# Optimization experiments

Hardware: AMD Instinct MI355X
Metric: run time of the kernel (lower is better)

The kernel has to match this reference:

```python
import jax, jax.numpy as jnp
import numpy as np
from jax import lax

DN = ('NCHW', 'OIHW', 'NCHW')


def convbn(x, w, s, b, relu=True):
    # conv (no bias) + folded BatchNorm affine (+ optional ReLU)
    y = lax.conv_general_dilated(x, w, (1, 1), 'SAME', dimension_numbers=DN)
    y = y * s[None, :, None, None] + b[None, :, None, None]
    return jnp.maximum(y, 0.0) if relu else y


_PARAM_SHAPES = [
    ('t', (128, 256, 3, 3)), ('l', (128, 256, 3, 3)),
    ('b', (128, 256, 3, 3)), ('r', (128, 256, 3, 3)),
    ('tl3', (256, 128, 3, 3)), ('br3', (256, 128, 3, 3)),
    ('tl1', (256, 256, 1, 1)), ('br1', (256, 256, 1, 1)),
    ('tlo', (256, 256, 3, 3)), ('bro', (256, 256, 3, 3)),
]


def setup_inputs() -> dict:
    key = jax.random.key(0)
    B, C, H, W = 8, 256, 128, 128
    ks = jax.random.split(key, 3 * len(_PARAM_SHAPES) + 1)
    inp = {'x': jax.random.normal(ks[0], (B, C, H, W), jnp.float32)}
    i = 1
    for name, shape in _PARAM_SHAPES:
        cout = shape[0]
        inp['w_' + name] = jax.random.normal(ks[i], shape, jnp.float32) * 0.05
        inp['s_' + name] = 1.0 + 0.1 * jax.random.normal(ks[i + 1], (cout,), jnp.float32)
        inp['b_' + name] = 0.1 * jax.random.normal(ks[i + 2], (cout,), jnp.float32)
        i += 3
    return inp


def reference(x, w_t, s_t, b_t, w_l, s_l, b_l, w_b, s_b, b_b, w_r, s_r, b_r,
              w_tl3, s_tl3, b_tl3, w_br3, s_br3, b_br3,
              w_tl1, s_tl1, b_tl1, w_br1, s_br1, b_br1,
              w_tlo, s_tlo, b_tlo, w_bro, s_bro, b_bro):
    # directional corner pools = (reverse-)cummax along H (axis 2) or W (axis 3)
    t = convbn(x, w_t, s_t, b_t)
    tp = lax.cummax(t, axis=2, reverse=True)   # top_pool: max over rows >= h
    l = convbn(x, w_l, s_l, b_l)
    lp = lax.cummax(l, axis=3, reverse=True)   # left_pool: max over cols >= w
    bo = convbn(x, w_b, s_b, b_b)
    bp = lax.cummax(bo, axis=2)                # bottom_pool: max over rows <= h
    r = convbn(x, w_r, s_r, b_r)
    rp = lax.cummax(r, axis=3)                 # right_pool: max over cols <= w

    tl = convbn(tp + lp, w_tl3, s_tl3, b_tl3, relu=False)
    tl = jnp.maximum(tl + convbn(x, w_tl1, s_tl1, b_tl1, relu=False), 0.0)
    out_tl = convbn(tl, w_tlo, s_tlo, b_tlo)

    br = convbn(bp + rp, w_br3, s_br3, b_br3, relu=False)
    br = jnp.maximum(br + convbn(x, w_br1, s_br1, b_br1, relu=False), 0.0)
    out_br = convbn(br, w_bro, s_bro, b_bro)
    return out_tl, out_br
```

## Files before the change

### kernel.cpp

```cpp
#include <hip/hip_runtime.h>
#include <cstdint>
#include <cstddef>


typedef float  f32x4 __attribute__((ext_vector_type(4)));
typedef float  f4v   __attribute__((ext_vector_type(4)));
typedef short  s16x8 __attribute__((ext_vector_type(8)));
typedef unsigned short u16x4 __attribute__((ext_vector_type(4)));

__device__ __forceinline__ float bf2f(unsigned short u) {
    unsigned x = ((unsigned)u) << 16;
    return __builtin_bit_cast(float, x);
}
__device__ __forceinline__ unsigned short f2bf(float f) {
    unsigned u = __builtin_bit_cast(unsigned, f);
    unsigned r = (u + 0x7fffu + ((u >> 16) & 1u)) >> 16;
    return (unsigned short)r;
}

#define GL_LDS(gp, lp) __builtin_amdgcn_global_load_lds( \
    (const __attribute__((address_space(1))) unsigned int*)(const void*)(gp), \
    (__attribute__((address_space(3))) unsigned int*)(void*)(lp), 16, 0, 0)

template<int CIN, int COUT, bool RELU, bool OUTF32, bool SWZ>
__global__ __launch_bounds__(256, 4)
void conv3_mfma(const unsigned short* __restrict__ in,
                const unsigned short* __restrict__ wpk,
                const float* __restrict__ sc, const float* __restrict__ bi,
                void* __restrict__ outv)
{
    __shared__ unsigned short lds[2][8704];
    const int tid  = threadIdx.x;
    const int lane = tid & 63;
    const int wv   = tid >> 6;
    const int c    = lane & 15;
    const int g    = lane >> 4;

    constexpr int GX  = (COUT / 128) * 2;
    int gx, hy, n;
    if (SWZ) {
        constexpr int NWG = GX * 64 * 8;
        constexpr int Q   = NWG / 8;
        const int braw = blockIdx.x + GX * (blockIdx.y + 64 * blockIdx.z);
        const int wl   = (braw & 7) * Q + (braw >> 3);
        gx = wl % GX;
        const int rest = wl / GX;
        hy = rest & 63;
        n  = rest >> 6;
    } else {
        gx = blockIdx.x; hy = blockIdx.y; n = blockIdx.z;
    }
    const int wtile  = gx & 1;
    const int octile = gx >> 1;
    const int h0   = hy * 2;
    const int w0   = wtile * 64;
    const int r    = wv >> 1;
    const int ocbase = octile * 128 + (wv & 1) * 64;
    const int ocf0   = octile * 8 + (wv & 1) * 4;

    int addrB[3];
    #pragma unroll
    for (int kx = 0; kx < 3; ++kx) {
        int ps0 = c + kx;
        addrB[kx] = r * 4224 + ps0 * 64 + ((g ^ ((ps0 >> 1) & 3)) << 4);
    }

    int so[5];
    #pragma unroll
    for (int it = 0; it < 5; ++it) {
        int u   = it * 256 + tid;
        int row = u / 264;
        int rem = u - row * 264;
        int ps  = rem >> 2;
        int s   = rem & 3;
        int icq = s ^ ((ps >> 1) & 3);
        so[it] = ((n * 130 + h0 + row) * 130 + (w0 + ps)) * CIN + icq * 8;
    }

    auto STAGE = [&](int chunk, int bsel) {
        const unsigned short* bp = in + chunk * 32;
        char* lb = (char*)lds + bsel * 17408 + tid * 16;
        #pragma unroll
        for (int it = 0; it < 4; ++it)
            GL_LDS(bp + so[it], lb + it * 4096);
        if (wv == 0)
            GL_LDS(bp + so[4], lb + 16384);
    };

    f32x4 acc[4][4];
    #pragma unroll
    for (int m = 0; m < 4; ++m)
        #pragma unroll
        for (int p = 0; p < 4; ++p) acc[m][p] = 0.0f;

    const int NC = CIN / 32;
    STAGE(0, 0);
    __syncthreads();

    for (int chunk = 0; chunk < NC; ++chunk) {
        const int cur = chunk & 1;
        if (chunk + 1 < NC) STAGE(chunk + 1, cur ^ 1);
        const char* lb = (const char*)lds + cur * 17408;
        #pragma unroll
        for (int kk = 0; kk < 9; ++kk) {
            const int ky = kk / 3, kx = kk % 3;
            s16x8 af[4], bf[4];
            #pragma unroll
            for (int m = 0; m < 4; ++m)
                af[m] = *(const s16x8*)(wpk
                    + ((size_t)((chunk * 9 + kk) * (COUT / 16) + ocf0 + m)) * 512 + lane * 8);
            #pragma unroll
            for (int p = 0; p < 4; ++p)
                bf[p] = *(const s16x8*)(lb + addrB[kx] + ky * 4224 + p * 1024);
            #pragma unroll
            for (int m = 0; m < 4; ++m)
                #pragma unroll
                for (int p = 0; p < 4; ++p)
                    acc[m][p] = __builtin_amdgcn_mfma_f32_16x16x32_bf16(af[m], bf[p], acc[m][p], 0, 0, 0);
        }
        __syncthreads();
    }

    #pragma unroll
    for (int m = 0; m < 4; ++m) {
        const int oc4 = ocbase + m * 16 + g * 4;
        const f4v s4 = *(const f4v*)(sc + oc4);
        const f4v b4 = *(const f4v*)(bi + oc4);
        #pragma unroll
        for (int p = 0; p < 4; ++p) {
            const int w = w0 + p * 16 + c;
            float y[4];
            #pragma unroll
            for (int j = 0; j < 4; ++j) {
                y[j] = acc[m][p][j] * s4[j] + b4[j];
                if (RELU) y[j] = fmaxf(y[j], 0.0f);
            }
            if (OUTF32) {
                float* op = (float*)outv + (((size_t)n * COUT + oc4) << 14) + ((h0 + r) << 7) + w;
                op[0] = y[0]; op[16384] = y[1]; op[32768] = y[2]; op[49152] = y[3];
            } else {
                u16x4 pk;
                #pragma unroll
                for (int j = 0; j < 4; ++j) pk[j] = f2bf(y[j]);
                *(u16x4*)((unsigned short*)outv
                    + ((size_t)(n * 130 + h0 + r + 1) * 130 + w + 1) * COUT + oc4) = pk;
            }
        }
    }
}

__global__ __launch_bounds__(256, 4)
void conv3_tlbr(const unsigned short* __restrict__ in,
                const unsigned short* __restrict__ wq0,
                const float* __restrict__ sA, const float* __restrict__ bA,
                unsigned short* __restrict__ tt0)
{
    __shared__ unsigned short lds[2][8704];
    const int tid  = threadIdx.x;
    const int lane = tid & 63;
    const int wv   = tid >> 6;
    const int c    = lane & 15;
    const int g    = lane >> 4;

    const int b  = blockIdx.x;
    const int x  = b & 7;
    const int t  = b >> 3;
    const int q  = t & 3;
    const int ts = x + 8 * (t >> 2);
    const int wtile = ts & 1;
    const int hy    = (ts >> 1) & 63;
    const int n     = ts >> 7;
    const int h0 = hy * 2;
    const int w0 = wtile * 64;
    const int r  = wv >> 1;
    const int ocbase = (wv & 1) * 64;
    const int ocf0   = (wv & 1) * 4;

    const unsigned short* wpk = wq0 + q * 294912;
    const int outoff = ((q & 1) << 1) | (q >> 1);
    unsigned short* outv = tt0 + (size_t)outoff * ((size_t)8 * 130 * 130 * 128);
    const float* sc = sA + q * 128;
    const float* bi = bA + q * 128;

    int addrB[3];
    #pragma unroll
    for (int kx = 0; kx < 3; ++kx) {
        int ps0 = c + kx;
        addrB[kx] = r * 4224 + ps0 * 64 + ((g ^ ((ps0 >> 1) & 3)) << 4);
    }

    int so[5];
    #pragma unroll
    for (int it = 0; it < 5; ++it) {
        int u   = it * 256 + tid;
        int row = u / 264;
        int rem = u - row * 264;
        int ps  = rem >> 2;
        int s   = rem & 3;
        int icq = s ^ ((ps >> 1) & 3);
        so[it] = ((n * 130 + h0 + row) * 130 + (w0 + ps)) * 256 + icq * 8;
    }

    auto STAGE = [&](int chunk, int bsel) {
        const unsigned short* bp = in + chunk * 32;
        char* lb = (char*)lds + bsel * 17408 + tid * 16;
        #pragma unroll
        for (int it = 0; it < 4; ++it)
            GL_LDS(bp + so[it], lb + it * 4096);
        if (wv == 0)
            GL_LDS(bp + so[4], lb + 16384);
    };

    f32x4 acc[4][4];
    #pragma unroll
    for (int m = 0; m < 4; ++m)
        #pragma unroll
        for (int p = 0; p < 4; ++p) acc[m][p] = 0.0f;

    STAGE(0, 0);
    __syncthreads();

    for (int chunk = 0; chunk < 8; ++chunk) {
        const int cur = chunk & 1;
        if (chunk + 1 < 8) STAGE(chunk + 1, cur ^ 1);
        const char* lb = (const char*)lds + cur * 17408;
        #pragma unroll
        for (int kk = 0; kk < 9; ++kk) {
            const int ky = kk / 3, kx = kk % 3;
            s16x8 af[4], bf[4];
            #pragma unroll
            for (int m = 0; m < 4; ++m)
                af[m] = *(const s16x8*)(wpk
                    + ((size_t)((chunk * 9 + kk) * 8 + ocf0 + m)) * 512 + lane * 8);
            #pragma unroll
            for (int p = 0; p < 4; ++p)
                bf[p] = *(const s16x8*)(lb + addrB[kx] + ky * 4224 + p * 1024);
            #pragma unroll
            for (int m = 0; m < 4; ++m)
                #pragma unroll
                for (int p = 0; p < 4; ++p)
                    acc[m][p] = __builtin_amdgcn_mfma_f32_16x16x32_bf16(af[m], bf[p], acc[m][p], 0, 0, 0);
        }
        __syncthreads();
    }

    #pragma unroll
    for (int m = 0; m < 4; ++m) {
        const int oc4 = ocbase + m * 16 + g * 4;
        const f4v s4 = *(const f4v*)(sc + oc4);
        const f4v b4 = *(const f4v*)(bi + oc4);
        #pragma unroll
        for (int p = 0; p < 4; ++p) {
            const int w = w0 + p * 16 + c;
            u16x4 pk;
            #pragma unroll
            for (int j = 0; j < 4; ++j)
                pk[j] = f2bf(fmaxf(acc[m][p][j] * s4[j] + b4[j], 0.0f));
            *(u16x4*)(outv + ((size_t)(n * 130 + h0 + r + 1) * 130 + w + 1) * 128 + oc4) = pk;
        }
    }
}

__global__ __launch_bounds__(256, 2)
void conv1_mfma(const unsigned short* __restrict__ xb,
                const unsigned short* __restrict__ w1pk,
                const float* __restrict__ sc, const float* __restrict__ bi,
                unsigned short* __restrict__ io)
{
    const int tid  = threadIdx.x;
    const int h    = blockIdx.y;
    const int n    = blockIdx.z;
    const int lane = tid & 63;
    const int wv   = tid >> 6;
    const int c    = lane & 15;
    const int g    = lane >> 4;
    const int pixbase = (wv >> 1) * 64;
    const int ocbase  = blockIdx.x * 128 + (wv & 1) * 64;
    const int ocf0    = blockIdx.x * 8 + (wv & 1) * 4;
    const size_t pixrow = ((size_t)(n * 130 + h + 1) * 130 + (pixbase + c + 1)) * 256;

    f32x4 acc[4][4];
    #pragma unroll
    for (int m = 0; m < 4; ++m)
        #pragma unroll
        for (int p = 0; p < 4; ++p) acc[m][p] = 0.0f;

    s16x8 a0[4], b0[4], a1[4], b1[4];

#define LOADC(ck, A, B) do {                                                        \
    _Pragma("unroll") for (int p = 0; p < 4; ++p)                                   \
        B[p] = *(const s16x8*)(xb + pixrow + (size_t)(16 * p) * 256 + (ck) * 32 + g * 8); \
    _Pragma("unroll") for (int m = 0; m < 4; ++m)                                   \
        A[m] = *(const s16x8*)(w1pk + ((size_t)((ck) * 16 + ocf0 + m)) * 512 + lane * 8); \
} while (0)
#define MM(A, B)                                                                    \
    _Pragma("unroll") for (int m = 0; m < 4; ++m)                                   \
        _Pragma("unroll") for (int p = 0; p < 4; ++p)                               \
            acc[m][p] = __builtin_amdgcn_mfma_f32_16x16x32_bf16(A[m], B[p], acc[m][p], 0, 0, 0)

    LOADC(0, a0, b0);
    #pragma unroll
    for (int ck = 0; ck < 8; ++ck) {
        if ((ck & 1) == 0) { if (ck < 7) LOADC(ck + 1, a1, b1); MM(a0, b0); }
        else               { if (ck < 7) LOADC(ck + 1, a0, b0); MM(a1, b1); }
    }
#undef LOADC
#undef MM

    #pragma unroll
    for (int m = 0; m < 4; ++m) {
        const int oc4 = ocbase + m * 16 + g * 4;
        const f4v s4 = *(const f4v*)(sc + oc4);
        const f4v b4 = *(const f4v*)(bi + oc4);
        #pragma unroll
        for (int p = 0; p < 4; ++p) {
            const int pix = pixbase + p * 16 + c;
            size_t idx = ((size_t)(n * 130 + h + 1) * 130 + pix + 1) * 256 + oc4;
            u16x4 old = *(const u16x4*)(io + idx);
            u16x4 pk;
            #pragma unroll
            for (int j = 0; j < 4; ++j) {
                float y = acc[m][p][j] * s4[j] + b4[j] + bf2f(old[j]);
                pk[j] = f2bf(fmaxf(y, 0.0f));
            }
            *(u16x4*)(io + idx) = pk;
        }
    }
}

__global__ __launch_bounds__(128)
void pool_h2_k(unsigned short* __restrict__ ta, unsigned short* __restrict__ tb)
{
    const int sel = blockIdx.x & 1;
    const int col = blockIdx.x >> 1;
    unsigned short* p = sel ? tb : ta;
    const int n = col >> 7, w = col & 127, cth = threadIdx.x;
    unsigned short* base = p + (((size_t)n * 130 + 1) * 130 + (w + 1)) * 128 + cth;
    const int stride = 130 * 128;
    float m = -3.402823466e+38f;
    if (sel == 0) {
        for (int gq = 0; gq < 16; ++gq) {
            const int h0 = 127 - gq * 8;
            float v[8];
            #pragma unroll
            for (int j = 0; j < 8; ++j) v[j] = bf2f(base[(size_t)(h0 - j) * stride]);
            unsigned short o[8];
            #pragma unroll
            for (int j = 0; j < 8; ++j) { m = fmaxf(m, v[j]); o[j] = f2bf(m); }
            #pragma unroll
            for (int j = 0; j < 8; ++j) base[(size_t)(h0 - j) * stride] = o[j];
        }
    } else {
        for (int gq = 0; gq < 16; ++gq) {
            const int h0 = gq * 8;
            float v[8];
            #pragma unroll
            for (int j = 0; j < 8; ++j) v[j] = bf2f(base[(size_t)(h0 + j) * stride]);
            unsigned short o[8];
            #pragma unroll
            for (int j = 0; j < 8; ++j) { m = fmaxf(m, v[j]); o[j] = f2bf(m); }
            #pragma unroll
            for (int j = 0; j < 8; ++j) base[(size_t)(h0 + j) * stride] = o[j];
        }
    }
}

__global__ __launch_bounds__(128)
void pool_w_add2_k(const unsigned short* __restrict__ la, unsigned short* __restrict__ ta,
                   const unsigned short* __restrict__ lb, unsigned short* __restrict__ tb)
{
    const int sel = blockIdx.x & 1;
    const int row = blockIdx.x >> 1;
    const unsigned short* ls = sel ? lb : la;
    unsigned short* td = sel ? tb : ta;
    const int n = row >> 7, hh = row & 127, cth = threadIdx.x;
    const size_t rowbase = ((size_t)(n * 130 + hh + 1) * 130) * 128 + cth;
    float m = -3.402823466e+38f;
    if (sel == 0) {
        for (int gq = 0; gq < 16; ++gq) {
            const int w0 = 127 - gq * 8;
            float lv[8], tv[8];
            #pragma unroll
            for (int j = 0; j < 8; ++j) {
                size_t off = rowbase + (size_t)(w0 - j + 1) * 128;
                lv[j] = bf2f(ls[off]); tv[j] = bf2f(td[off]);
            }
            unsigned short o[8];
            #pragma unroll
            for (int j = 0; j < 8; ++j) { m = fmaxf(m, lv[j]); o[j] = f2bf(m + tv[j]); }
            #pragma unroll
            for (int j = 0; j < 8; ++j) td[rowbase + (size_t)(w0 - j + 1) * 128] = o[j];
        }
    } else {
        for (int gq = 0; gq < 16; ++gq) {
            const int w0 = gq * 8;
            float lv[8], tv[8];
            #pragma unroll
            for (int j = 0; j < 8; ++j) {
                size_t off = rowbase + (size_t)(w0 + j + 1) * 128;
                lv[j] = bf2f(ls[off]); tv[j] = bf2f(td[off]);
            }
            unsigned short o[8];
            #pragma unroll
            for (int j = 0; j < 8; ++j) { m = fmaxf(m, lv[j]); o[j] = f2bf(m + tv[j]); }
            #pragma unroll
            for (int j = 0; j < 8; ++j) td[rowbase + (size_t)(w0 + j + 1) * 128] = o[j];
        }
    }
}

__global__ __launch_bounds__(256)
void padzero_k(unsigned short* __restrict__ t, int C)
{
    int idx = blockIdx.x * 256 + threadIdx.x;
    int n = blockIdx.y;
    int cpu = C >> 3;
    if (idx >= 516 * cpu) return;
    int cell = idx / cpu, cq = idx - cell * cpu;
    int h, w;
    if (cell < 260) { h = (cell < 130) ? -1 : 128; w = (cell % 130) - 1; }
    else { int j = cell - 260; w = (j < 128) ? -1 : 128; h = j & 127; }
    size_t off = (((size_t)n * 130 + h + 1) * 130 + (w + 1)) * C + cq * 8;
    uint4 z; z.x = 0; z.y = 0; z.z = 0; z.w = 0;
    *(uint4*)(t + off) = z;
}

__global__ __launch_bounds__(256)
void padzero_all_k(unsigned short* xb, unsigned short* tt, unsigned short* bb,
                   unsigned short* ll, unsigned short* rr)
{
    const int id = blockIdx.y;
    unsigned short* t = id == 0 ? xb : (id == 1 ? tt : (id == 2 ? bb : (id == 3 ? ll : rr)));
    const int C = id == 0 ? 256 : 128;
    int idx = blockIdx.x * 256 + threadIdx.x;
    int n = blockIdx.z;
    int cpu = C >> 3;
    if (idx >= 516 * cpu) return;
    int cell = idx / cpu, cq = idx - cell * cpu;
    int h, w;
    if (cell < 260) { h = (cell < 130) ? -1 : 128; w = (cell % 130) - 1; }
    else { int j = cell - 260; w = (j < 128) ? -1 : 128; h = j & 127; }
    size_t off = (((size_t)n * 130 + h + 1) * 130 + (w + 1)) * C + cq * 8;
    uint4 z; z.x = 0; z.y = 0; z.z = 0; z.w = 0;
    *(uint4*)(t + off) = z;
}

__global__ __launch_bounds__(256)
void transform_x_k(const float* __restrict__ x, unsigned short* __restrict__ xb)
{
    __shared__ float sm[64][132];
    const int h = blockIdx.x, n = blockIdx.y, t = threadIdx.x;
    for (int cc0 = 0; cc0 < 256; cc0 += 64) {
        __syncthreads();
        {
            int ci = t >> 7, wi = t & 127;
            #pragma unroll 8
            for (int k = 0; k < 32; ++k)
                sm[ci + 2 * k][wi] = x[((size_t)(n * 256 + cc0 + ci + 2 * k) << 14) + (h << 7) + wi];
        }
        __syncthreads();
        {
            int wi = t >> 1, cq = t & 1;
            unsigned short tmp[32];
            #pragma unroll
            for (int m2 = 0; m2 < 32; ++m2) tmp[m2] = f2bf(sm[cq * 32 + m2][wi]);
            unsigned short* dst = xb + (((size_t)n * 130 + h + 1) * 130 + wi + 1) * 256 + cc0 + cq * 32;
            #pragma unroll
            for (int q = 0; q < 4; ++q) *(uint4*)(dst + q * 8) = *(const uint4*)(tmp + q * 8);
        }
    }
}

struct PrepArgs {
    const float* w[10];
    unsigned short* dst[10];
    const float* sv[4];
    const float* bv[4];
    float* sA; float* bA;
};

__global__ __launch_bounds__(256)
void prepack_all_k(PrepArgs a)
{
    const int id = blockIdx.y;
    int idx = blockIdx.x * 256 + threadIdx.x;
    if (id == 10) {
        if (idx < 512) {
            a.sA[idx] = a.sv[idx >> 7][idx & 127];
            a.bA[idx] = a.bv[idx >> 7][idx & 127];
        }
        return;
    }
    if (id >= 8) {
        if (idx >= 65536) return;
        int ic = idx & 255, oc = idx >> 8;
        float v = a.w[id][oc * 256 + ic];
        int chunk = ic >> 5, icr = ic & 31, gg = icr >> 3, j = icr & 7;
        int m = oc >> 4, ocr = oc & 15, ln = gg * 16 + ocr;
        a.dst[id][((size_t)(chunk * 16 + m)) * 512 + ln * 8 + j] = f2bf(v);
        return;
    }
    const int CIN  = (id < 4) ? 256 : ((id < 6) ? 128 : 256);
    const int COUT = (id < 4) ? 128 : 256;
    if (idx >= COUT * CIN * 9) return;
    int kk = idx % 9; int rest = idx / 9;
    int ic = rest % CIN; int oc = rest / CIN;
    float v = a.w[id][(size_t)(oc * CIN + ic) * 9 + kk];
    int chunk = ic >> 5, icr = ic & 31, gg = icr >> 3, j = icr & 7;
    int m = oc >> 4, ocr = oc & 15, ln = gg * 16 + ocr;
    a.dst[id][((size_t)((chunk * 9 + kk) * (COUT / 16) + m)) * 512 + ln * 8 + j] = f2bf(v);
}

extern "C" void kernel_launch(void* const* d_in, const int* in_sizes, int n_in,
                              void* d_out, int out_size, void* d_ws, size_t ws_size,
                              hipStream_t stream)
{
    const float* x     = (const float*)d_in[0];
    const float* w_t   = (const float*)d_in[1];
    const float* s_t   = (const float*)d_in[2];
    const float* b_t   = (const float*)d_in[3];
    const float* w_l   = (const float*)d_in[4];
    const float* s_l   = (const float*)d_in[5];
    const float* b_l   = (const float*)d_in[6];
    const float* w_b   = (const float*)d_in[7];
    const float* s_b   = (const float*)d_in[8];
    const float* b_b   = (const float*)d_in[9];
    const float* w_r   = (const float*)d_in[10];
    const float* s_r   = (const float*)d_in[11];
    const float* b_r   = (const float*)d_in[12];
    const float* w_tl3 = (const float*)d_in[13];
    const float* s_tl3 = (const float*)d_in[14];
    const float* b_tl3 = (const float*)d_in[15];
    const float* w_br3 = (const float*)d_in[16];
    const float* s_br3 = (const float*)d_in[17];
    const float* b_br3 = (const float*)d_in[18];
    const float* w_tl1 = (const float*)d_in[19];
    const float* s_tl1 = (const float*)d_in[20];
    const float* b_tl1 = (const float*)d_in[21];
    const float* w_br1 = (const float*)d_in[22];
    const float* s_br1 = (const float*)d_in[23];
    const float* b_br1 = (const float*)d_in[24];
    const float* w_tlo = (const float*)d_in[25];
    const float* s_tlo = (const float*)d_in[26];
    const float* b_tlo = (const float*)d_in[27];
    const float* w_bro = (const float*)d_in[28];
    const float* s_bro = (const float*)d_in[29];
    const float* b_bro = (const float*)d_in[30];

    typedef unsigned short ush;
    const size_t T256 = (size_t)8 * 130 * 130 * 256;
    const size_t T128 = (size_t)8 * 130 * 130 * 128;

    ush* xb = (ush*)d_ws;
    ush* tt = xb + T256;
    ush* bb = tt + T128;
    ush* ll = bb + T128;
    ush* rr = ll + T128;
    ush* wq = rr + T128;
    ush* wp_t   = wq;
    ush* wp_l   = wp_t   + 294912;
    ush* wp_b   = wp_l   + 294912;
    ush* wp_r   = wp_b   + 294912;
    ush* wp_tl3 = wp_r   + 294912;
    ush* wp_br3 = wp_tl3 + 294912;
    ush* wp_tlo = wp_br3 + 294912;
    ush* wp_bro = wp_tlo + 589824;
    ush* wp_tl1 = wp_bro + 589824;
    ush* wp_br1 = wp_tl1 + 65536;
    float* sA   = (float*)(wp_br1 + 65536);
    float* bA   = sA + 512;
    ush* tl = ll;

    PrepArgs pa;
    pa.w[0] = w_t;  pa.w[1] = w_l;  pa.w[2] = w_b;  pa.w[3] = w_r;
    pa.w[4] = w_tl3; pa.w[5] = w_br3; pa.w[6] = w_tlo; pa.w[7] = w_bro;
    pa.w[8] = w_tl1; pa.w[9] = w_br1;
    pa.dst[0] = wp_t;  pa.dst[1] = wp_l;  pa.dst[2] = wp_b;  pa.dst[3] = wp_r;
    pa.dst[4] = wp_tl3; pa.dst[5] = wp_br3; pa.dst[6] = wp_tlo; pa.dst[7] = wp_bro;
    pa.dst[8] = wp_tl1; pa.dst[9] = wp_br1;
    pa.sv[0] = s_t; pa.sv[1] = s_l; pa.sv[2] = s_b; pa.sv[3] = s_r;
    pa.bv[0] = b_t; pa.bv[1] = b_l; pa.bv[2] = b_b; pa.bv[3] = b_r;
    pa.sA = sA; pa.bA = bA;
    prepack_all_k<<<dim3(2304, 11), dim3(256), 0, stream>>>(pa);
    padzero_all_k<<<dim3(516, 5, 8), dim3(256), 0, stream>>>(xb, tt, bb, ll, rr);
    transform_x_k<<<dim3(128, 8), dim3(256), 0, stream>>>(x, xb);

    conv3_tlbr<<<dim3(4096), dim3(256), 0, stream>>>(xb, wp_t, sA, bA, tt);

    pool_h2_k<<<dim3(2048), dim3(128), 0, stream>>>(tt, bb);
    pool_w_add2_k<<<dim3(2048), dim3(128), 0, stream>>>(ll, tt, rr, bb);

    padzero_k<<<dim3(66, 8), dim3(256), 0, stream>>>(tl, 256);
    conv3_mfma<128, 256, false, false, true><<<dim3(4, 64, 8), dim3(256), 0, stream>>>(tt, wp_tl3, s_tl3, b_tl3, tl);
    conv1_mfma<<<dim3(2, 128, 8), dim3(256), 0, stream>>>(xb, wp_tl1, s_tl1, b_tl1, tl);
    conv3_mfma<256, 256, true, true, true><<<dim3(4, 64, 8), dim3(256), 0, stream>>>(tl, wp_tlo, s_tlo, b_tlo, d_out);

    conv3_mfma<128, 256, false, false, true><<<dim3(4, 64, 8), dim3(256), 0, stream>>>(bb, wp_br3, s_br3, b_br3, tl);
    conv1_mfma<<<dim3(2, 128, 8), dim3(256), 0, stream>>>(xb, wp_br1, s_br1, b_br1, tl);
    conv3_mfma<256, 256, true, true, true><<<dim3(4, 64, 8), dim3(256), 0, stream>>>(tl, wp_bro, s_bro, b_bro,
                                                                                     (float*)d_out + 33554432);
}
```

Baseline: 924.8 us.

## Fuse 3x3 and 1x1 residual convs into one kernel for both branches, fold BN scale

Folds the BatchNorm scale into the packed weights and pre-sums the tl3/tl1 and br3/br1 biases, so epilogues only add a bias. The tl3+tl1 and br3+br1 convolutions are merged into a single kernel that accumulates both GEMMs in registers, handles both branches in one launch, and stages the 1x1 input through LDS. The BR intermediate is stored in the output buffer so both branches can run in that one launch. The aim is to drop the read-modify-write of the intermediate, two launches, and the scale loads. The catch is the extra prepack work and relying on the output buffer as scratch being ordered correctly (bro is run first).

```diff
diff --git a/kernel.cpp b/kernel.cpp
--- a/kernel.cpp
+++ b/kernel.cpp
@@ -26,7 +26,7 @@
 __global__ __launch_bounds__(256, 4)
 void conv3_mfma(const unsigned short* __restrict__ in,
                 const unsigned short* __restrict__ wpk,
-                const float* __restrict__ sc, const float* __restrict__ bi,
+                const float* __restrict__ bi,
                 void* __restrict__ outv)
 {
     __shared__ unsigned short lds[2][8704];
@@ -124,7 +124,6 @@
     #pragma unroll
     for (int m = 0; m < 4; ++m) {
         const int oc4 = ocbase + m * 16 + g * 4;
-        const f4v s4 = *(const f4v*)(sc + oc4);
         const f4v b4 = *(const f4v*)(bi + oc4);
         #pragma unroll
         for (int p = 0; p < 4; ++p) {
@@ -132,7 +131,7 @@
             float y[4];
             #pragma unroll
             for (int j = 0; j < 4; ++j) {
-                y[j] = acc[m][p][j] * s4[j] + b4[j];
+                y[j] = acc[m][p][j] + b4[j];
                 if (RELU) y[j] = fmaxf(y[j], 0.0f);
             }
             if (OUTF32) {
@@ -152,7 +151,7 @@
 __global__ __launch_bounds__(256, 4)
 void conv3_tlbr(const unsigned short* __restrict__ in,
                 const unsigned short* __restrict__ wq0,
-                const float* __restrict__ sA, const float* __restrict__ bA,
+                const float* __restrict__ bA,
                 unsigned short* __restrict__ tt0)
 {
     __shared__ unsigned short lds[2][8704];
@@ -179,7 +178,6 @@
     const unsigned short* wpk = wq0 + q * 294912;
     const int outoff = ((q & 1) << 1) | (q >> 1);
     unsigned short* outv = tt0 + (size_t)outoff * ((size_t)8 * 130 * 130 * 128);
-    const float* sc = sA + q * 128;
     const float* bi = bA + q * 128;
 
     int addrB[3];
@@ -247,7 +245,6 @@
     #pragma unroll
     for (int m = 0; m < 4; ++m) {
         const int oc4 = ocbase + m * 16 + g * 4;
-        const f4v s4 = *(const f4v*)(sc + oc4);
         const f4v b4 = *(const f4v*)(bi + oc4);
         #pragma unroll
         for (int p = 0; p < 4; ++p) {
@@ -255,29 +252,99 @@
             u16x4 pk;
             #pragma unroll
             for (int j = 0; j < 4; ++j)
-                pk[j] = f2bf(fmaxf(acc[m][p][j] * s4[j] + b4[j], 0.0f));
+                pk[j] = f2bf(fmaxf(acc[m][p][j] + b4[j], 0.0f));
             *(u16x4*)(outv + ((size_t)(n * 130 + h0 + r + 1) * 130 + w + 1) * 128 + oc4) = pk;
         }
     }
 }
 
-__global__ __launch_bounds__(256, 2)
-void conv1_mfma(const unsigned short* __restrict__ xb,
-                const unsigned short* __restrict__ w1pk,
-                const float* __restrict__ sc, const float* __restrict__ bi,
-                unsigned short* __restrict__ io)
-{
+__global__ __launch_bounds__(256, 4)
+void conv3p1_k(const unsigned short* __restrict__ u0,
+               const unsigned short* __restrict__ xb,
+               const unsigned short* __restrict__ w30,
+               const unsigned short* __restrict__ w10,
+               const float* __restrict__ bsum0,
+               unsigned short* __restrict__ outTL,
+               unsigned short* __restrict__ outBR)
+{
+    __shared__ unsigned short lds[2][8704];
     const int tid  = threadIdx.x;
-    const int h    = blockIdx.y;
-    const int n    = blockIdx.z;
     const int lane = tid & 63;
     const int wv   = tid >> 6;
     const int c    = lane & 15;
     const int g    = lane >> 4;
-    const int pixbase = (wv >> 1) * 64;
-    const int ocbase  = blockIdx.x * 128 + (wv & 1) * 64;
-    const int ocf0    = blockIdx.x * 8 + (wv & 1) * 4;
-    const size_t pixrow = ((size_t)(n * 130 + h + 1) * 130 + (pixbase + c + 1)) * 256;
+
+    const int b  = blockIdx.x;
+    const int x  = b & 7;
+    const int s  = b >> 3;
+    const int q  = s & 1;
+    const int gx = (s >> 1) & 3;
+    const int sp = x + 8 * (s >> 3);
+    const int hy = sp & 63;
+    const int n  = sp >> 6;
+    const int wtile  = gx & 1;
+    const int octile = gx >> 1;
+    const int h0 = hy * 2;
+    const int w0 = wtile * 64;
+    const int r  = wv >> 1;
+    const int ocbase = octile * 128 + (wv & 1) * 64;
+    const int ocf0   = octile * 8 + (wv & 1) * 4;
+
+    const unsigned short* in3 = u0 + (size_t)q * ((size_t)8 * 130 * 130 * 128);
+    const unsigned short* w3  = w30 + q * 294912;
+    const unsigned short* w1  = w10 + q * 65536;
+    const float* bi = bsum0 + q * 256;
+    unsigned short* outv = q ? outBR : outTL;
+
+    int addrB[3];
+    #pragma unroll
+    for (int kx = 0; kx < 3; ++kx) {
+        int ps0 = c + kx;
+        addrB[kx] = r * 4224 + ps0 * 64 + ((g ^ ((ps0 >> 1) & 3)) << 4);
+    }
+    const int addrC1 = r * 4096 + c * 64 + ((g ^ ((c >> 1) & 3)) << 4);
+
+    int so3[5];
+    #pragma unroll
+    for (int it = 0; it < 5; ++it) {
+        int u   = it * 256 + tid;
+        int row = u / 264;
+        int rem = u - row * 264;
+        int ps  = rem >> 2;
+        int ss  = rem & 3;
+        int icq = ss ^ ((ps >> 1) & 3);
+        so3[it] = ((n * 130 + h0 + row) * 130 + (w0 + ps)) * 128 + icq * 8;
+    }
+    int so1[4];
+    #pragma unroll
+    for (int it = 0; it < 4; ++it) {
+        int u   = it * 256 + tid;
+        int sub = u >> 9;
+        int v   = u & 511;
+        int row = v >> 8;
+        int rem = v & 255;
+        int px  = rem >> 2;
+        int ss  = rem & 3;
+        int icq = ss ^ ((px >> 1) & 3);
+        so1[it] = ((n * 130 + h0 + 1 + row) * 130 + (w0 + px + 1)) * 256 + sub * 32 + icq * 8;
+    }
+
+    auto STAGE3 = [&](int chunk, int bsel) {
+        const unsigned short* bp = in3 + chunk * 32;
+        char* lb = (char*)lds + bsel * 17408 + tid * 16;
+        #pragma unroll
+        for (int it = 0; it < 4; ++it)
+            GL_LDS(bp + so3[it], lb + it * 4096);
+        if (wv == 0)
+            GL_LDS(bp + so3[4], lb + 16384);
+    };
+    auto STAGE1 = [&](int j, int bsel) {
+        const unsigned short* bp = xb + j * 64;
+        char* lb = (char*)lds + bsel * 17408 + tid * 16;
+        #pragma unroll
+        for (int it = 0; it < 4; ++it)
+            GL_LDS(bp + so1[it], lb + it * 4096);
+    };
 
     f32x4 acc[4][4];
     #pragma unroll
@@ -285,45 +352,66 @@
         #pragma unroll
         for (int p = 0; p < 4; ++p) acc[m][p] = 0.0f;
 
-    s16x8 a0[4], b0[4], a1[4], b1[4];
-
-#define LOADC(ck, A, B) do {                                                        \
-    _Pragma("unroll") for (int p = 0; p < 4; ++p)                                   \
-        B[p] = *(const s16x8*)(xb + pixrow + (size_t)(16 * p) * 256 + (ck) * 32 + g * 8); \
-    _Pragma("unroll") for (int m = 0; m < 4; ++m)                                   \
-        A[m] = *(const s16x8*)(w1pk + ((size_t)((ck) * 16 + ocf0 + m)) * 512 + lane * 8); \
-} while (0)
-#define MM(A, B)                                                                    \
-    _Pragma("unroll") for (int m = 0; m < 4; ++m)                                   \
-        _Pragma("unroll") for (int p = 0; p < 4; ++p)                               \
-            acc[m][p] = __builtin_amdgcn_mfma_f32_16x16x32_bf16(A[m], B[p], acc[m][p], 0, 0, 0)
-
-    LOADC(0, a0, b0);
-    #pragma unroll
-    for (int ck = 0; ck < 8; ++ck) {
-        if ((ck & 1) == 0) { if (ck < 7) LOADC(ck + 1, a1, b1); MM(a0, b0); }
-        else               { if (ck < 7) LOADC(ck + 1, a0, b0); MM(a1, b1); }
-    }
-#undef LOADC
-#undef MM
+    STAGE3(0, 0);
+    __syncthreads();
+
+    for (int ph = 0; ph < 8; ++ph) {
+        const int cur = ph & 1;
+        if (ph < 3)      STAGE3(ph + 1, cur ^ 1);
+        else if (ph < 7) STAGE1(ph - 3, cur ^ 1);
+        const char* lb = (const char*)lds + cur * 17408;
+        if (ph < 4) {
+            #pragma unroll
+            for (int kk = 0; kk < 9; ++kk) {
+                const int ky = kk / 3, kx = kk % 3;
+                s16x8 af[4], bf[4];
+                #pragma unroll
+                for (int m = 0; m < 4; ++m)
+                    af[m] = *(const s16x8*)(w3
+                        + ((size_t)((ph * 9 + kk) * 16 + ocf0 + m)) * 512 + lane * 8);
+                #pragma unroll
+                for (int p = 0; p < 4; ++p)
+                    bf[p] = *(const s16x8*)(lb + addrB[kx] + ky * 4224 + p * 1024);
+                #pragma unroll
+                for (int m = 0; m < 4; ++m)
+                    #pragma unroll
+                    for (int p = 0; p < 4; ++p)
+                        acc[m][p] = __builtin_amdgcn_mfma_f32_16x16x32_bf16(af[m], bf[p], acc[m][p], 0, 0, 0);
+            }
+        } else {
+            const int j = ph - 4;
+            #pragma unroll
+            for (int sub = 0; sub < 2; ++sub) {
+                s16x8 af[4], bf[4];
+                #pragma unroll
+                for (int m = 0; m < 4; ++m)
+                    af[m] = *(const s16x8*)(w1
+                        + ((size_t)(((j * 2 + sub) * 16) + ocf0 + m)) * 512 + lane * 8);
+                #pragma unroll
+                for (int p = 0; p < 4; ++p)
+                    bf[p] = *(const s16x8*)(lb + sub * 8192 + addrC1 + p * 1024);
+                #pragma unroll
+                for (int m = 0; m < 4; ++m)
+                    #pragma unroll
+                    for (int p = 0; p < 4; ++p)
+                        acc[m][p] = __builtin_amdgcn_mfma_f32_16x16x32_bf16(af[m], bf[p], acc[m][p], 0, 0, 0);
+            }
+        }
+        __syncthreads();
+    }
 
     #pragma unroll
     for (int m = 0; m < 4; ++m) {
         const int oc4 = ocbase + m * 16 + g * 4;
-        const f4v s4 = *(const f4v*)(sc + oc4);
         const f4v b4 = *(const f4v*)(bi + oc4);
         #pragma unroll
         for (int p = 0; p < 4; ++p) {
-            const int pix = pixbase + p * 16 + c;
-            size_t idx = ((size_t)(n * 130 + h + 1) * 130 + pix + 1) * 256 + oc4;
-            u16x4 old = *(const u16x4*)(io + idx);
+            const int w = w0 + p * 16 + c;
             u16x4 pk;
             #pragma unroll
-            for (int j = 0; j < 4; ++j) {
-                float y = acc[m][p][j] * s4[j] + b4[j] + bf2f(old[j]);
-                pk[j] = f2bf(fmaxf(y, 0.0f));
-            }
-            *(u16x4*)(io + idx) = pk;
+            for (int j = 0; j < 4; ++j)
+                pk[j] = f2bf(fmaxf(acc[m][p][j] + b4[j], 0.0f));
+            *(u16x4*)(outv + ((size_t)(n * 130 + h0 + r + 1) * 130 + w + 1) * 256 + oc4) = pk;
         }
     }
 }
@@ -427,11 +515,12 @@
 
 __global__ __launch_bounds__(256)
 void padzero_all_k(unsigned short* xb, unsigned short* tt, unsigned short* bb,
-                   unsigned short* ll, unsigned short* rr)
+                   unsigned short* ll, unsigned short* rr, unsigned short* pbr)
 {
     const int id = blockIdx.y;
-    unsigned short* t = id == 0 ? xb : (id == 1 ? tt : (id == 2 ? bb : (id == 3 ? ll : rr)));
-    const int C = id == 0 ? 256 : 128;
+    unsigned short* t = id == 0 ? xb : (id == 1 ? tt : (id == 2 ? bb :
+                        (id == 3 ? ll : (id == 4 ? rr : pbr))));
+    const int C = (id == 0 || id == 5) ? 256 : 128;
     int idx = blockIdx.x * 256 + threadIdx.x;
     int n = blockIdx.z;
     int cpu = C >> 3;
@@ -474,9 +563,10 @@
 struct PrepArgs {
     const float* w[10];
     unsigned short* dst[10];
-    const float* sv[4];
+    const float* s[10];
     const float* bv[4];
-    float* sA; float* bA;
+    const float* bx[4];
+    float* bA; float* bsum;
 };
 
 __global__ __launch_bounds__(256)
@@ -485,16 +575,15 @@
     const int id = blockIdx.y;
     int idx = blockIdx.x * 256 + threadIdx.x;
     if (id == 10) {
-        if (idx < 512) {
-            a.sA[idx] = a.sv[idx >> 7][idx & 127];
-            a.bA[idx] = a.bv[idx >> 7][idx & 127];
-        }
+        if (idx < 512) a.bA[idx] = a.bv[idx >> 7][idx & 127];
+        else if (idx < 768)  { int i = idx - 512; a.bsum[i]       = a.bx[0][i] + a.bx[1][i]; }
+        else if (idx < 1024) { int i = idx - 768; a.bsum[256 + i] = a.bx[2][i] + a.bx[3][i]; }
         return;
     }
     if (id >= 8) {
         if (idx >= 65536) return;
         int ic = idx & 255, oc = idx >> 8;
-        float v = a.w[id][oc * 256 + ic];
+        float v = a.w[id][oc * 256 + ic] * a.s[id][oc];
         int chunk = ic >> 5, icr = ic & 31, gg = icr >> 3, j = icr & 7;
         int m = oc >> 4, ocr = oc & 15, ln = gg * 16 + ocr;
         a.dst[id][((size_t)(chunk * 16 + m)) * 512 + ln * 8 + j] = f2bf(v);
@@ -505,7 +594,7 @@
     if (idx >= COUT * CIN * 9) return;
     int kk = idx % 9; int rest = idx / 9;
     int ic = rest % CIN; int oc = rest / CIN;
-    float v = a.w[id][(size_t)(oc * CIN + ic) * 9 + kk];
+    float v = a.w[id][(size_t)(oc * CIN + ic) * 9 + kk] * a.s[id][oc];
     int chunk = ic >> 5, icr = ic & 31, gg = icr >> 3, j = icr & 7;
     int m = oc >> 4, ocr = oc & 15, ln = gg * 16 + ocr;
     a.dst[id][((size_t)((chunk * 9 + kk) * (COUT / 16) + m)) * 512 + ln * 8 + j] = f2bf(v);
@@ -567,9 +656,10 @@
     ush* wp_bro = wp_tlo + 589824;
     ush* wp_tl1 = wp_bro + 589824;
     ush* wp_br1 = wp_tl1 + 65536;
-    float* sA   = (float*)(wp_br1 + 65536);
-    float* bA   = sA + 512;
-    ush* tl = ll;
+    float* bA   = (float*)(wp_br1 + 65536);
+    float* bsum = bA + 512;
+    ush* tl  = ll;
+    ush* pbr = (ush*)d_out;
 
     PrepArgs pa;
     pa.w[0] = w_t;  pa.w[1] = w_l;  pa.w[2] = w_b;  pa.w[3] = w_r;
@@ -578,25 +668,26 @@
     pa.dst[0] = wp_t;  pa.dst[1] = wp_l;  pa.dst[2] = wp_b;  pa.dst[3] = wp_r;
     pa.dst[4] = wp_tl3; pa.dst[5] = wp_br3; pa.dst[6] = wp_tlo; pa.dst[7] = wp_bro;
     pa.dst[8] = wp_tl1; pa.dst[9] = wp_br1;
-    pa.sv[0] = s_t; pa.sv[1] = s_l; pa.sv[2] = s_b; pa.sv[3] = s_r;
+    pa.s[0] = s_t;  pa.s[1] = s_l;  pa.s[2] = s_b;  pa.s[3] = s_r;
+    pa.s[4] = s_tl3; pa.s[5] = s_br3; pa.s[6] = s_tlo; pa.s[7] = s_bro;
+    pa.s[8] = s_tl1; pa.s[9] = s_br1;
     pa.bv[0] = b_t; pa.bv[1] = b_l; pa.bv[2] = b_b; pa.bv[3] = b_r;
-    pa.sA = sA; pa.bA = bA;
+    pa.bx[0] = b_tl3; pa.bx[1] = b_tl1; pa.bx[2] = b_br3; pa.bx[3] = b_br1;
+    pa.bA = bA; pa.bsum = bsum;
     prepack_all_k<<<dim3(2304, 11), dim3(256), 0, stream>>>(pa);
-    padzero_all_k<<<dim3(516, 5, 8), dim3(256), 0, stream>>>(xb, tt, bb, ll, rr);
+    padzero_all_k<<<dim3(516, 6, 8), dim3(256), 0, stream>>>(xb, tt, bb, ll, rr, pbr);
     transform_x_k<<<dim3(128, 8), dim3(256), 0, stream>>>(x, xb);
 
-    conv3_tlbr<<<dim3(4096), dim3(256), 0, stream>>>(xb, wp_t, sA, bA, tt);
+    conv3_tlbr<<<dim3(4096), dim3(256), 0, stream>>>(xb, wp_t, bA, tt);
 
     pool_h2_k<<<dim3(2048), dim3(128), 0, stream>>>(tt, bb);
     pool_w_add2_k<<<dim3(2048), dim3(128), 0, stream>>>(ll, tt, rr, bb);
 
     padzero_k<<<dim3(66, 8), dim3(256), 0, stream>>>(tl, 256);
-    conv3_mfma<128, 256, false, false, true><<<dim3(4, 64, 8), dim3(256), 0, stream>>>(tt, wp_tl3, s_tl3, b_tl3, tl);
-    conv1_mfma<<<dim3(2, 128, 8), dim3(256), 0, stream>>>(xb, wp_tl1, s_tl1, b_tl1, tl);
-    conv3_mfma<256, 256, true, true, true><<<dim3(4, 64, 8), dim3(256), 0, stream>>>(tl, wp_tlo, s_tlo, b_tlo, d_out);
-
-    conv3_mfma<128, 256, false, false, true><<<dim3(4, 64, 8), dim3(256), 0, stream>>>(bb, wp_br3, s_br3, b_br3, tl);
-    conv1_mfma<<<dim3(2, 128, 8), dim3(256), 0, stream>>>(xb, wp_br1, s_br1, b_br1, tl);
-    conv3_mfma<256, 256, true, true, true><<<dim3(4, 64, 8), dim3(256), 0, stream>>>(tl, wp_bro, s_bro, b_bro,
-                                                                                     (float*)d_out + 33554432);
-}
+    conv3p1_k<<<dim3(4096), dim3(256), 0, stream>>>(tt, xb, wp_tl3, wp_tl1, bsum, tl, pbr);
+
+    conv3_mfma<256, 256, true, true, true><<<dim3(4, 64, 8), dim3(256), 0, stream>>>(
+        pbr, wp_bro, b_bro, (float*)d_out + 33554432);
+    conv3_mfma<256, 256, true, true, true><<<dim3(4, 64, 8), dim3(256), 0, stream>>>(
+        tl, wp_tlo, b_tlo, d_out);
+}
```

After: 873.5 us (median of 2 runs). 1.06x faster.
